# Kernel optimization log

Hardware: AMD Instinct MI355X
Metric: run time of the kernel (lower is better)

Reference implementation:

```python
import jax, jax.numpy as jnp
import numpy as np

DROP_P = 0.1
REG = 0.01

NU, NI, D, B = 12000, 16000, 64, 1024


def setup_inputs() -> dict:
    key = jax.random.key(0)
    ks = jax.random.split(key, 10)
    return {
        "L_u": jax.random.normal(ks[0], (NU, NU), dtype=jnp.float32),
        "L_i": jax.random.normal(ks[1], (NI, NI), dtype=jnp.float32),
        "user_embed": jax.random.normal(ks[2], (NU, D), dtype=jnp.float32),
        "item_embed": jax.random.normal(ks[3], (NI, D), dtype=jnp.float32),
        "mask_u": jax.random.uniform(ks[4], (B, NU), dtype=jnp.float32),
        "mask_p": jax.random.uniform(ks[5], (B, NI), dtype=jnp.float32),
        "mask_n": jax.random.uniform(ks[6], (B, NI), dtype=jnp.float32),
        "user": jax.random.randint(ks[7], (B,), 0, NU),
        "pos_item": jax.random.randint(ks[8], (B,), 0, NI),
        "nega_item": jax.random.randint(ks[9], (B,), 0, NI),
    }


def reference(L_u, L_i, user_embed, item_embed, mask_u, mask_p, mask_n, user, pos_item, nega_item):
    # torch Dropout scales by 1/(1-p); code multiplies back by (1-p) -> net binary mask.
    keep_u = (mask_u >= DROP_P).astype(L_u.dtype)
    keep_p = (mask_p >= DROP_P).astype(L_i.dtype)
    keep_n = (mask_n >= DROP_P).astype(L_i.dtype)

    # gather filter rows, mask, project through embedding table: [B, N] @ [N, D]
    final_user = (L_u[user] * keep_u) @ user_embed        # [B, D]
    final_pos = (L_i[pos_item] * keep_p) @ item_embed    # [B, D]
    final_nega = (L_i[nega_item] * keep_n) @ item_embed  # [B, D]

    res_nega = jnp.sum(final_user * final_nega, axis=1)  # [B]
    nega_weight = jax.lax.stop_gradient(
        1.0 - jnp.log10(1.0 - jnp.minimum(jax.nn.sigmoid(res_nega), 0.99))
    )
    out = jax.nn.sigmoid(jnp.sum(final_user * final_pos, axis=1) - nega_weight * res_nega)

    reg_term = REG * (jnp.sum(final_user ** 2) + jnp.sum(final_pos ** 2) + jnp.sum(final_nega ** 2))
    batch = user.shape[0]
    return (-jnp.sum(jnp.log(out)) + reg_term) / batch
```

## Files before the change

kernel.cpp:

```cpp
#include <hip/hip_runtime.h>
#include <math.h>

#define NU_ 12000
#define NI_ 16000
#define NPU 12288
#define NPI 16384
#define DD 64
#define BB 1024
#define KC 256
#define SPL 8

typedef unsigned short ushort_t;
typedef __bf16 bf16x8 __attribute__((ext_vector_type(8)));
typedef float  f32x4  __attribute__((ext_vector_type(4)));
typedef unsigned short ushort4v __attribute__((ext_vector_type(4)));

static __device__ __forceinline__ ushort_t f2bf(float f) {
    __bf16 h = (__bf16)f;
    return __builtin_bit_cast(unsigned short, h);
}

__global__ __launch_bounds__(256) void gde_transpose(
    const float* __restrict__ E, ushort_t* __restrict__ Et, int N, int Np)
{
    __shared__ ushort_t Ls[64][65];
    const int n0  = blockIdx.x * 64;
    const int tid = threadIdx.x;
    const int dg  = tid & 15;
    const int nr  = tid >> 4;
#pragma unroll
    for (int nn = 0; nn < 4; ++nn) {
        const int nl = nn * 16 + nr;
        const int n  = n0 + nl;
        float4 v = make_float4(0.f, 0.f, 0.f, 0.f);
        if (n < N) v = *(const float4*)(E + (size_t)n * DD + dg * 4);
        Ls[nl][dg * 4 + 0] = f2bf(v.x);
        Ls[nl][dg * 4 + 1] = f2bf(v.y);
        Ls[nl][dg * 4 + 2] = f2bf(v.z);
        Ls[nl][dg * 4 + 3] = f2bf(v.w);
    }
    __syncthreads();
    const int d   = tid & 63;
    const int nl0 = (tid >> 6) * 16;
#pragma unroll
    for (int g = 0; g < 4; ++g) {
        ushort4v t;
#pragma unroll
        for (int i = 0; i < 4; ++i) t[i] = Ls[nl0 + g * 4 + i][d];
        *(ushort4v*)(Et + (size_t)d * Np + n0 + nl0 + g * 4) = t;
    }
}

__global__ __launch_bounds__(256, 2) void gde_gemm(
    const float* __restrict__ L_u, const float* __restrict__ L_i,
    const ushort_t* __restrict__ EtU, const ushort_t* __restrict__ EtI,
    const float* __restrict__ mu,  const float* __restrict__ mp,
    const float* __restrict__ mn,
    const int* __restrict__ user, const int* __restrict__ pos,
    const int* __restrict__ nega,
    float* __restrict__ P, int S)
{
    __shared__ ushort_t As[32 * 256];

    const int rt  = blockIdx.x;
    const int s   = blockIdx.y;
    const int j   = blockIdx.z;
    const int tid = threadIdx.x;
    const int w   = tid >> 6;
    const int l   = tid & 63;

    const float* L; const ushort_t* Et; const float* M; const int* idx;
    int N, Np;
    if (j == 0)      { L = L_u; Et = EtU; M = mu; idx = user; N = NU_; Np = NPU; }
    else if (j == 1) { L = L_i; Et = EtI; M = mp; idx = pos;  N = NI_; Np = NPI; }
    else             { L = L_i; Et = EtI; M = mn; idx = nega; N = NI_; Np = NPI; }

    const int base = rt * 32;
    unsigned int Loff[8], Moff[8];
#pragma unroll
    for (int r = 0; r < 8; ++r) {
        const int row = base + w * 8 + r;
        Loff[r] = (unsigned int)idx[row] * (unsigned int)(N * 4);
        Moff[r] = (unsigned int)row * (unsigned int)(N * 4);
    }

    const int dcol = l & 15;
    const int g4   = l >> 4;
    const ushort_t* Eb[4];
#pragma unroll
    for (int df = 0; df < 4; ++df) Eb[df] = Et + (size_t)(df * 16 + dcol) * Np;

    f32x4 acc[8];
#pragma unroll
    for (int i = 0; i < 8; ++i) acc[i] = (f32x4){0.f, 0.f, 0.f, 0.f};

    const int nc  = (N + KC - 1) / KC;
    const int kb0 = (s * nc) / S;
    const int kb1 = ((s + 1) * nc) / S;

    float4 La[8], Ma[8];
#pragma unroll
    for (int r = 0; r < 8; ++r) { La[r] = make_float4(0.f,0.f,0.f,0.f); Ma[r] = La[r]; }

    {
        const int kg = kb0 * KC + 4 * l;
        const size_t boff = (size_t)kg * 4u;
        if (kg < N) {
#pragma unroll
            for (int r = 0; r < 8; ++r) {
                La[r] = *(const float4*)((const char*)L + Loff[r] + boff);
                Ma[r] = *(const float4*)((const char*)M + Moff[r] + boff);
            }
        }
    }

    for (int kb = kb0; kb < kb1; ++kb) {
#pragma unroll
        for (int r = 0; r < 8; ++r) {
            const int row = w * 8 + r;
            ushort4v t;
            t[0] = (Ma[r].x >= 0.1f) ? f2bf(La[r].x) : (ushort_t)0;
            t[1] = (Ma[r].y >= 0.1f) ? f2bf(La[r].y) : (ushort_t)0;
            t[2] = (Ma[r].z >= 0.1f) ? f2bf(La[r].z) : (ushort_t)0;
            t[3] = (Ma[r].w >= 0.1f) ? f2bf(La[r].w) : (ushort_t)0;
            *(ushort4v*)((char*)As + (row << 9) + ((l * 8) ^ ((row & 7) << 4))) = t;
        }

        bf16x8 bfr[2][4];
#pragma unroll
        for (int h = 0; h < 2; ++h) {
            const int kk = kb * KC + (2 * w + h) * 32 + 8 * g4;
#pragma unroll
            for (int df = 0; df < 4; ++df)
                bfr[h][df] = *(const bf16x8*)(Eb[df] + kk);
        }
        asm volatile("" ::: "memory");

        if (kb + 1 < kb1) {
            const int kg = (kb + 1) * KC + 4 * l;
            const size_t boff = (size_t)kg * 4u;
            if (kg < N) {
#pragma unroll
                for (int r = 0; r < 8; ++r) {
                    La[r] = *(const float4*)((const char*)L + Loff[r] + boff);
                    Ma[r] = *(const float4*)((const char*)M + Moff[r] + boff);
                }
            }
        }

        asm volatile("s_waitcnt lgkmcnt(0)" ::: "memory");
        __builtin_amdgcn_s_barrier();
        asm volatile("" ::: "memory");

#pragma unroll
        for (int h = 0; h < 2; ++h) {
            const int ks = 2 * w + h;
            const int cb = 64 * ks + 16 * g4;
            const int r0 = dcol, r1 = 16 + dcol;
            const bf16x8 af0 = *(const bf16x8*)((char*)As + (r0 << 9) + (cb ^ ((r0 & 7) << 4)));
            const bf16x8 af1 = *(const bf16x8*)((char*)As + (r1 << 9) + (cb ^ ((r1 & 7) << 4)));
            acc[0] = __builtin_amdgcn_mfma_f32_16x16x32_bf16(af0, bfr[h][0], acc[0], 0, 0, 0);
            acc[1] = __builtin_amdgcn_mfma_f32_16x16x32_bf16(af0, bfr[h][1], acc[1], 0, 0, 0);
            acc[2] = __builtin_amdgcn_mfma_f32_16x16x32_bf16(af0, bfr[h][2], acc[2], 0, 0, 0);
            acc[3] = __builtin_amdgcn_mfma_f32_16x16x32_bf16(af0, bfr[h][3], acc[3], 0, 0, 0);
            acc[4] = __builtin_amdgcn_mfma_f32_16x16x32_bf16(af1, bfr[h][0], acc[4], 0, 0, 0);
            acc[5] = __builtin_amdgcn_mfma_f32_16x16x32_bf16(af1, bfr[h][1], acc[5], 0, 0, 0);
            acc[6] = __builtin_amdgcn_mfma_f32_16x16x32_bf16(af1, bfr[h][2], acc[6], 0, 0, 0);
            acc[7] = __builtin_amdgcn_mfma_f32_16x16x32_bf16(af1, bfr[h][3], acc[7], 0, 0, 0);
        }

        asm volatile("" ::: "memory");
        __builtin_amdgcn_s_barrier();
        asm volatile("" ::: "memory");
    }

    float* Pb = P + ((size_t)(j * (S * 4) + s * 4 + w) * BB + base) * DD;
#pragma unroll
    for (int ri = 0; ri < 4; ++ri) {
        const int m = g4 * 4 + ri;
        Pb[(size_t)m * DD +  0 + dcol] = acc[0][ri];
        Pb[(size_t)m * DD + 16 + dcol] = acc[1][ri];
        Pb[(size_t)m * DD + 32 + dcol] = acc[2][ri];
        Pb[(size_t)m * DD + 48 + dcol] = acc[3][ri];
        Pb[(size_t)(m + 16) * DD +  0 + dcol] = acc[4][ri];
        Pb[(size_t)(m + 16) * DD + 16 + dcol] = acc[5][ri];
        Pb[(size_t)(m + 16) * DD + 32 + dcol] = acc[6][ri];
        Pb[(size_t)(m + 16) * DD + 48 + dcol] = acc[7][ri];
    }
}

__global__ __launch_bounds__(256) void gde_finalize(
    const float* __restrict__ P, int Seff,
    float* __restrict__ term, float* __restrict__ regp)
{
    const int b    = blockIdx.x * 4 + (threadIdx.x >> 6);
    const int lane = threadIdx.x & 63;
    const size_t joff = (size_t)Seff * BB * DD;

    float fu = 0.f, fp_ = 0.f, fn = 0.f;
    for (int s = 0; s < Seff; ++s) {
        const size_t base = ((size_t)s * BB + b) * DD + lane;
        fu  += P[base];
        fp_ += P[base + joff];
        fn  += P[base + 2 * joff];
    }

    float rp = fu * fp_;
    float rn = fu * fn;
    float rg = fu * fu + fp_ * fp_ + fn * fn;
#pragma unroll
    for (int o = 32; o > 0; o >>= 1) {
        rp += __shfl_xor(rp, o);
        rn += __shfl_xor(rn, o);
        rg += __shfl_xor(rg, o);
    }

    if (lane == 0) {
        const float sn = 1.0f / (1.0f + expf(-rn));
        const float w  = 1.0f - log10f(1.0f - fminf(sn, 0.99f));
        const float x  = rp - w * rn;
        const float t  = -x;
        term[b] = fmaxf(t, 0.0f) + log1pf(expf(-fabsf(t)));
        regp[b] = rg;
    }
}

__global__ __launch_bounds__(256) void gde_reduce(
    const float* __restrict__ term, const float* __restrict__ regp,
    float* __restrict__ out)
{
    __shared__ float sm[256];
    const int t = threadIdx.x;
    float v = 0.f;
    for (int i = t; i < BB; i += 256)
        v += term[i] + 0.01f * regp[i];
    sm[t] = v;
    __syncthreads();
    for (int o = 128; o > 0; o >>= 1) {
        if (t < o) sm[t] += sm[t + o];
        __syncthreads();
    }
    if (t == 0) out[0] = sm[0] / (float)BB;
}

extern "C" void kernel_launch(void* const* d_in, const int* in_sizes, int n_in,
                              void* d_out, int out_size, void* d_ws, size_t ws_size,
                              hipStream_t stream)
{
    const float* L_u = (const float*)d_in[0];
    const float* L_i = (const float*)d_in[1];
    const float* ue  = (const float*)d_in[2];
    const float* ie  = (const float*)d_in[3];
    const float* mu  = (const float*)d_in[4];
    const float* mp  = (const float*)d_in[5];
    const float* mn  = (const float*)d_in[6];
    const int* user  = (const int*)d_in[7];
    const int* pos   = (const int*)d_in[8];
    const int* nega  = (const int*)d_in[9];
    float* out = (float*)d_out;

    const size_t etU_b  = (size_t)DD * NPU * 2;
    const size_t etI_b  = (size_t)DD * NPI * 2;
    const size_t slice  = (size_t)3 * BB * DD * 4;
    const size_t fixed  = etU_b + etI_b + 2 * BB * 4 + 256;
    int S = SPL;
    while (S > 1 && (size_t)(4 * S) * slice + fixed > ws_size) --S;
    const int Seff = 4 * S;

    float*    P    = (float*)d_ws;
    ushort_t* EtU  = (ushort_t*)((char*)d_ws + (size_t)Seff * slice);
    ushort_t* EtI  = (ushort_t*)((char*)EtU + etU_b);
    float*    term = (float*)((char*)EtI + etI_b);
    float*    regp = term + BB;

    gde_transpose<<<dim3(NPU / 64), dim3(256), 0, stream>>>(ue, EtU, NU_, NPU);
    gde_transpose<<<dim3(NPI / 64), dim3(256), 0, stream>>>(ie, EtI, NI_, NPI);

    gde_gemm<<<dim3(32, S, 3), dim3(256), 0, stream>>>(
        L_u, L_i, EtU, EtI, mu, mp, mn, user, pos, nega, P, S);

    gde_finalize<<<dim3(BB / 4), dim3(256), 0, stream>>>(P, Seff, term, regp);
    gde_reduce<<<dim3(1), dim3(256), 0, stream>>>(term, regp, out);
}
```

Measured before the change: 102.1 us.

## Pre-pack dropout masks into bitmaps before the masked GEMM

Adds a streaming kernel that thresholds each float dropout mask and packs eight keep flags into one byte. The GEMM then loads one byte per lane per row instead of a float4 of mask values, which frees registers, so the launch bound goes from 2 to 3 blocks per SM for higher occupancy. The full mask tensors are still read every call, now in a separate pass, so total memory traffic stays about the same. The change adds a kernel launch and a small bitmap write/read in exchange for a lighter GEMM inner loop.

```diff
diff --git a/kernel.cpp b/kernel.cpp
--- a/kernel.cpp
+++ b/kernel.cpp
@@ -10,6 +10,10 @@
 #define KC 256
 #define SPL 8
 
+#define MBU_ (BB * (NU_ / 8))
+#define MBI_ (BB * (NI_ / 8))
+#define MB_TOTAL (MBU_ + 2 * MBI_)
+
 typedef unsigned short ushort_t;
 typedef __bf16 bf16x8 __attribute__((ext_vector_type(8)));
 typedef float  f32x4  __attribute__((ext_vector_type(4)));
@@ -18,6 +22,33 @@
 static __device__ __forceinline__ ushort_t f2bf(float f) {
     __bf16 h = (__bf16)f;
     return __builtin_bit_cast(unsigned short, h);
+}
+
+__global__ __launch_bounds__(256) void gde_pack(
+    const float* __restrict__ mu, const float* __restrict__ mp,
+    const float* __restrict__ mn, unsigned char* __restrict__ Mb)
+{
+    const int j = blockIdx.y;
+    const float* src; size_t nb, off;
+    if (j == 0)      { src = mu; nb = MBU_; off = 0; }
+    else if (j == 1) { src = mp; nb = MBI_; off = MBU_; }
+    else             { src = mn; nb = MBI_; off = MBU_ + MBI_; }
+    unsigned char* dst = Mb + off;
+    const size_t stride = (size_t)gridDim.x * 256;
+    for (size_t i = (size_t)blockIdx.x * 256 + threadIdx.x; i < nb; i += stride) {
+        const float4 v0 = *(const float4*)(src + 8 * i);
+        const float4 v1 = *(const float4*)(src + 8 * i + 4);
+        unsigned int b = 0;
+        b |= (v0.x >= 0.1f) ?   1u : 0u;
+        b |= (v0.y >= 0.1f) ?   2u : 0u;
+        b |= (v0.z >= 0.1f) ?   4u : 0u;
+        b |= (v0.w >= 0.1f) ?   8u : 0u;
+        b |= (v1.x >= 0.1f) ?  16u : 0u;
+        b |= (v1.y >= 0.1f) ?  32u : 0u;
+        b |= (v1.z >= 0.1f) ?  64u : 0u;
+        b |= (v1.w >= 0.1f) ? 128u : 0u;
+        dst[i] = (unsigned char)b;
+    }
 }
 
 __global__ __launch_bounds__(256) void gde_transpose(
@@ -51,11 +82,10 @@
     }
 }
 
-__global__ __launch_bounds__(256, 2) void gde_gemm(
+__global__ __launch_bounds__(256, 3) void gde_gemm(
     const float* __restrict__ L_u, const float* __restrict__ L_i,
     const ushort_t* __restrict__ EtU, const ushort_t* __restrict__ EtI,
-    const float* __restrict__ mu,  const float* __restrict__ mp,
-    const float* __restrict__ mn,
+    const unsigned char* __restrict__ Mb,
     const int* __restrict__ user, const int* __restrict__ pos,
     const int* __restrict__ nega,
     float* __restrict__ P, int S)
@@ -69,19 +99,19 @@
     const int w   = tid >> 6;
     const int l   = tid & 63;
 
-    const float* L; const ushort_t* Et; const float* M; const int* idx;
+    const float* L; const ushort_t* Et; const unsigned char* MbB; const int* idx;
     int N, Np;
-    if (j == 0)      { L = L_u; Et = EtU; M = mu; idx = user; N = NU_; Np = NPU; }
-    else if (j == 1) { L = L_i; Et = EtI; M = mp; idx = pos;  N = NI_; Np = NPI; }
-    else             { L = L_i; Et = EtI; M = mn; idx = nega; N = NI_; Np = NPI; }
+    if (j == 0)      { L = L_u; Et = EtU; MbB = Mb;               idx = user; N = NU_; Np = NPU; }
+    else if (j == 1) { L = L_i; Et = EtI; MbB = Mb + MBU_;        idx = pos;  N = NI_; Np = NPI; }
+    else             { L = L_i; Et = EtI; MbB = Mb + MBU_ + MBI_; idx = nega; N = NI_; Np = NPI; }
 
     const int base = rt * 32;
-    unsigned int Loff[8], Moff[8];
+    unsigned int Loff[8], Boff[8];
 #pragma unroll
     for (int r = 0; r < 8; ++r) {
         const int row = base + w * 8 + r;
         Loff[r] = (unsigned int)idx[row] * (unsigned int)(N * 4);
-        Moff[r] = (unsigned int)row * (unsigned int)(N * 4);
+        Boff[r] = (unsigned int)row * (unsigned int)(N / 8);
     }
 
     const int dcol = l & 15;
@@ -98,31 +128,35 @@
     const int kb0 = (s * nc) / S;
     const int kb1 = ((s + 1) * nc) / S;
 
-    float4 La[8], Ma[8];
-#pragma unroll
-    for (int r = 0; r < 8; ++r) { La[r] = make_float4(0.f,0.f,0.f,0.f); Ma[r] = La[r]; }
+    float4 La[8];
+    unsigned int mbv[8];
+#pragma unroll
+    for (int r = 0; r < 8; ++r) { La[r] = make_float4(0.f,0.f,0.f,0.f); mbv[r] = 0; }
 
     {
         const int kg = kb0 * KC + 4 * l;
-        const size_t boff = (size_t)kg * 4u;
         if (kg < N) {
+            const size_t boff = (size_t)kg * 4u;
+            const unsigned int moff = (unsigned int)(kb0 * KC / 8 + (l >> 1));
 #pragma unroll
             for (int r = 0; r < 8; ++r) {
-                La[r] = *(const float4*)((const char*)L + Loff[r] + boff);
-                Ma[r] = *(const float4*)((const char*)M + Moff[r] + boff);
+                La[r]  = *(const float4*)((const char*)L + Loff[r] + boff);
+                mbv[r] = MbB[Boff[r] + moff];
             }
         }
     }
 
     for (int kb = kb0; kb < kb1; ++kb) {
+        const unsigned int sh = (l & 1) << 2;
 #pragma unroll
         for (int r = 0; r < 8; ++r) {
             const int row = w * 8 + r;
+            const unsigned int bits = mbv[r] >> sh;
             ushort4v t;
-            t[0] = (Ma[r].x >= 0.1f) ? f2bf(La[r].x) : (ushort_t)0;
-            t[1] = (Ma[r].y >= 0.1f) ? f2bf(La[r].y) : (ushort_t)0;
-            t[2] = (Ma[r].z >= 0.1f) ? f2bf(La[r].z) : (ushort_t)0;
-            t[3] = (Ma[r].w >= 0.1f) ? f2bf(La[r].w) : (ushort_t)0;
+            t[0] = (bits & 1u) ? f2bf(La[r].x) : (ushort_t)0;
+            t[1] = (bits & 2u) ? f2bf(La[r].y) : (ushort_t)0;
+            t[2] = (bits & 4u) ? f2bf(La[r].z) : (ushort_t)0;
+            t[3] = (bits & 8u) ? f2bf(La[r].w) : (ushort_t)0;
             *(ushort4v*)((char*)As + (row << 9) + ((l * 8) ^ ((row & 7) << 4))) = t;
         }
 
@@ -138,12 +172,13 @@
 
         if (kb + 1 < kb1) {
             const int kg = (kb + 1) * KC + 4 * l;
-            const size_t boff = (size_t)kg * 4u;
             if (kg < N) {
+                const size_t boff = (size_t)kg * 4u;
+                const unsigned int moff = (unsigned int)((kb + 1) * KC / 8 + (l >> 1));
 #pragma unroll
                 for (int r = 0; r < 8; ++r) {
-                    La[r] = *(const float4*)((const char*)L + Loff[r] + boff);
-                    Ma[r] = *(const float4*)((const char*)M + Moff[r] + boff);
+                    La[r]  = *(const float4*)((const char*)L + Loff[r] + boff);
+                    mbv[r] = MbB[Boff[r] + moff];
                 }
             }
         }
@@ -262,22 +297,24 @@
     const size_t etU_b  = (size_t)DD * NPU * 2;
     const size_t etI_b  = (size_t)DD * NPI * 2;
     const size_t slice  = (size_t)3 * BB * DD * 4;
-    const size_t fixed  = etU_b + etI_b + 2 * BB * 4 + 256;
+    const size_t fixed  = etU_b + etI_b + MB_TOTAL + 2 * BB * 4 + 512;
     int S = SPL;
     while (S > 1 && (size_t)(4 * S) * slice + fixed > ws_size) --S;
     const int Seff = 4 * S;
 
-    float*    P    = (float*)d_ws;
-    ushort_t* EtU  = (ushort_t*)((char*)d_ws + (size_t)Seff * slice);
-    ushort_t* EtI  = (ushort_t*)((char*)EtU + etU_b);
-    float*    term = (float*)((char*)EtI + etI_b);
-    float*    regp = term + BB;
-
+    float*         P    = (float*)d_ws;
+    ushort_t*      EtU  = (ushort_t*)((char*)d_ws + (size_t)Seff * slice);
+    ushort_t*      EtI  = (ushort_t*)((char*)EtU + etU_b);
+    unsigned char* Mb   = (unsigned char*)((char*)EtI + etI_b);
+    float*         term = (float*)((char*)Mb + ((MB_TOTAL + 255) & ~255ull));
+    float*         regp = term + BB;
+
+    gde_pack<<<dim3(2048, 3), dim3(256), 0, stream>>>(mu, mp, mn, Mb);
     gde_transpose<<<dim3(NPU / 64), dim3(256), 0, stream>>>(ue, EtU, NU_, NPU);
     gde_transpose<<<dim3(NPI / 64), dim3(256), 0, stream>>>(ie, EtI, NI_, NPI);
 
     gde_gemm<<<dim3(32, S, 3), dim3(256), 0, stream>>>(
-        L_u, L_i, EtU, EtI, mu, mp, mn, user, pos, nega, P, S);
+        L_u, L_i, EtU, EtI, Mb, user, pos, nega, P, S);
 
     gde_finalize<<<dim3(BB / 4), dim3(256), 0, stream>>>(P, Seff, term, regp);
     gde_reduce<<<dim3(1), dim3(256), 0, stream>>>(term, regp, out);
```

Result: slower. 108.2 us (+6.0%).
